# Kernel tuning notes

Hardware: AMD Instinct MI355X
Metric: run time of the kernel (lower is better)

Reference implementation:

```python
import jax, jax.numpy as jnp
import numpy as np

EMBED_DIM = 2048
NUM_HEADS = 16
HEAD_DIM = EMBED_DIM // NUM_HEADS


def setup_inputs() -> dict:
    key = jax.random.key(0)
    k1, k2, k3, k4 = jax.random.split(key, 4)
    x = jax.random.normal(k1, (4, 2048, EMBED_DIM), dtype=jnp.float32)
    # torch nn.Linear weight shape: [out_features, in_features]
    W_qkv = jax.random.normal(k2, (3 * EMBED_DIM, EMBED_DIM), dtype=jnp.float32) * (EMBED_DIM ** -0.5)
    W_out = jax.random.normal(k3, (EMBED_DIM, EMBED_DIM), dtype=jnp.float32) * (EMBED_DIM ** -0.5)
    b_out = jax.random.normal(k4, (EMBED_DIM,), dtype=jnp.float32) * 0.01
    return {"x": x, "W_qkv": W_qkv, "W_out": W_out, "b_out": b_out}


def reference(x, W_qkv, W_out, b_out):
    B, S, E = x.shape
    H, D = NUM_HEADS, HEAD_DIM
    qkv = jnp.einsum('bse,fe->bsf', x, W_qkv)            # [B,S,3E]
    q, k, v = jnp.split(qkv, 3, axis=-1)
    # [B,S,E] -> [B,H,S,D]
    q = q.reshape(B, S, H, D).transpose(0, 2, 1, 3)
    k = k.reshape(B, S, H, D).transpose(0, 2, 1, 3)
    v = v.reshape(B, S, H, D).transpose(0, 2, 1, 3)
    scale = D ** -0.5
    scores = jnp.einsum('bhqd,bhkd->bhqk', q, k) * scale  # [B,H,S,S]
    attn = jax.nn.softmax(scores, axis=-1)
    out = jnp.einsum('bhqk,bhkd->bhqd', attn, v)          # [B,H,S,D]
    out = out.transpose(0, 2, 1, 3).reshape(B, S, E)
    return jnp.einsum('bse,fe->bsf', out, W_out) + b_out
```

## Files before the change

### kernel.cpp

```cpp
#include <hip/hip_runtime.h>
#include <stdint.h>
#include <stddef.h>

#define BATCH 4
#define SEQ   2048
#define EDIM  2048
#define NH    16
#define HD    128
#define MTOT  (BATCH*SEQ)

#define QSCALE (0.08838834764831845f * 1.4426950408889634f)

typedef __bf16 bf16_t;
typedef __attribute__((ext_vector_type(8))) __bf16 bf16x8;
typedef __attribute__((ext_vector_type(4))) __bf16 bf16x4;
typedef __attribute__((ext_vector_type(4))) float f32x4;
typedef __attribute__((ext_vector_type(16))) float f32x16;
typedef __attribute__((ext_vector_type(2))) unsigned int uint32x2;

#define GLD16(l, g) __builtin_amdgcn_global_load_lds( \
    (const uint32_t __attribute__((address_space(1)))*)(g), \
    (uint32_t __attribute__((address_space(3)))*)(l), 16, 0, 0)

#define RAW_BARRIER()  asm volatile("s_barrier" ::: "memory")
#define WAITCNT_VM(n)  asm volatile("s_waitcnt vmcnt(" #n ")" ::: "memory")

__global__ void cast_bf16_kernel(const float* __restrict__ in,
                                 bf16_t* __restrict__ out, int n4) {
    int i = blockIdx.x * blockDim.x + threadIdx.x;
    if (i < n4) {
        float4 v = ((const float4*)in)[i];
        bf16x4 o = { (__bf16)v.x, (__bf16)v.y, (__bf16)v.z, (__bf16)v.w };
        ((bf16x4*)out)[i] = o;
    }
}

template<int EPI>
__global__ __launch_bounds__(256)
void gemm_nt(const bf16_t* __restrict__ A, const bf16_t* __restrict__ B,
             int M, int N, int K,
             float* __restrict__ outf, const float* __restrict__ bias,
             bf16_t* __restrict__ qb, bf16_t* __restrict__ kb,
             bf16_t* __restrict__ vb)
{
    __shared__ bf16_t As[128*64];
    __shared__ bf16_t Bs[128*64];
    const int tid  = threadIdx.x;
    const int lane = tid & 63;
    const int l15  = lane & 15;
    const int quad = lane >> 4;
    const int wave = tid >> 6;
    const int wm = (wave & 1) * 64;
    const int wn = (wave >> 1) * 64;
    const int bm = blockIdx.x * 128;
    const int bn = blockIdx.y * 128;

    f32x4 acc[4][4] = {};

    for (int k0 = 0; k0 < K; k0 += 64) {
#pragma unroll
        for (int i = 0; i < 4; i++) {
            int lin = i*2048 + tid*8;
            int row = lin >> 6;
            int c   = (lin >> 3) & 7;
            int scol = (c ^ (row & 7)) * 8;
            GLD16(&As[lin], A + (long)(bm + row)*K + k0 + scol);
            GLD16(&Bs[lin], B + (long)(bn + row)*K + k0 + scol);
        }
        __syncthreads();
#pragma unroll
        for (int kk = 0; kk < 2; kk++) {
            bf16x8 af[4], bfr[4];
#pragma unroll
            for (int mt = 0; mt < 4; mt++)
                af[mt] = *(const bf16x8*)&As[(wm + mt*16 + l15)*64 +
                                             (((kk*4 + quad) ^ (l15 & 7)) * 8)];
#pragma unroll
            for (int nt = 0; nt < 4; nt++)
                bfr[nt] = *(const bf16x8*)&Bs[(wn + nt*16 + l15)*64 +
                                              (((kk*4 + quad) ^ (l15 & 7)) * 8)];
#pragma unroll
            for (int mt = 0; mt < 4; mt++)
#pragma unroll
                for (int nt = 0; nt < 4; nt++)
                    acc[mt][nt] = __builtin_amdgcn_mfma_f32_16x16x32_bf16(
                        af[mt], bfr[nt], acc[mt][nt], 0, 0, 0);
        }
        __syncthreads();
    }

    if (EPI == 0) {
#pragma unroll
        for (int nt = 0; nt < 4; nt++) {
            int colg = bn + wn + nt*16 + l15;
            int which = colg >> 11;
            int e = colg & 2047;
            int h = e >> 7, d = e & 127;
#pragma unroll
            for (int mt = 0; mt < 4; mt++) {
#pragma unroll
                for (int r = 0; r < 4; r++) {
                    int rowg = bm + wm + mt*16 + quad*4 + r;
                    int b = rowg >> 11, s = rowg & 2047;
                    long bh = (long)b*NH + h;
                    if (which == 0)
                        qb[(bh*SEQ + s)*HD + d] = (__bf16)(acc[mt][nt][r] * QSCALE);
                    else if (which == 1)
                        kb[(bh*SEQ + s)*HD + d] = (__bf16)acc[mt][nt][r];
                    else
                        vb[(bh*HD + d)*SEQ + s] = (__bf16)acc[mt][nt][r];
                }
            }
        }
    } else {
#pragma unroll
        for (int nt = 0; nt < 4; nt++) {
            int colg = bn + wn + nt*16 + l15;
            float bv = bias[colg];
#pragma unroll
            for (int mt = 0; mt < 4; mt++)
#pragma unroll
                for (int r = 0; r < 4; r++) {
                    int rowg = bm + wm + mt*16 + quad*4 + r;
                    outf[(long)rowg*EDIM + colg] = acc[mt][nt][r] + bv;
                }
        }
    }
}

__device__ __forceinline__ void pswap(uint32_t& x, uint32_t& y) {
    uint32x2 r = __builtin_amdgcn_permlane32_swap(x, y, false, false);
    x = r[0]; y = r[1];
}
__device__ __forceinline__ uint32_t pkbf16(float a, float b) {
    union { uint32_t u; __bf16 h[2]; } w;
    w.h[0] = (__bf16)a; w.h[1] = (__bf16)b;
    return w.u;
}
__device__ __forceinline__ float xswap_max(float v) {
    union { float f; uint32_t u; } a, b;
    a.f = v; b.f = v;
    pswap(a.u, b.u);
    return fmaxf(a.f, b.f);
}
__device__ __forceinline__ float xswap_add(float v) {
    union { float f; uint32_t u; } a, b;
    a.f = v; b.f = v;
    pswap(a.u, b.u);
    return a.f + b.f;
}

template<int B>
__device__ __forceinline__ bf16x8 mkfrag(f32x16 p) {
    uint32_t w0 = pkbf16(p[B+0], p[B+1]);
    uint32_t w2 = pkbf16(p[B+4], p[B+5]);
    pswap(w0, w2);
    uint32_t w1 = pkbf16(p[B+2], p[B+3]);
    uint32_t w3 = pkbf16(p[B+6], p[B+7]);
    pswap(w1, w3);
    union { uint32_t u[4]; bf16x8 v; } r;
    r.u[0] = w0; r.u[1] = w1; r.u[2] = w2; r.u[3] = w3;
    return r.v;
}

__global__ __launch_bounds__(512, 2)
void attn_kernel(const bf16_t* __restrict__ qb, const bf16_t* __restrict__ kb,
                 const bf16_t* __restrict__ vb, bf16_t* __restrict__ ob)
{
    __shared__ bf16_t SM[32768];
    bf16_t* const K0 = SM;
    bf16_t* const K1 = SM + 8192;
    bf16_t* const V0 = SM + 16384;
    bf16_t* const V1 = SM + 24576;

    const int tid  = threadIdx.x;
    const int lane = tid & 63;
    const int l31  = lane & 31;
    const int l15  = lane & 15;
    const int l7   = lane & 7;
    const int hi   = lane >> 5;
    const int warp = tid >> 6;

    const int bh = blockIdx.x & 63;
    const int q0 = (blockIdx.x >> 6) * 256;
    const int b  = bh >> 4;
    const int h  = bh & 15;

    const bf16_t* kg0 = kb + (long)bh*SEQ*HD;
    const bf16_t* vg0 = vb + (long)bh*HD*SEQ;

    bf16x8 qf[8];
    {
        const bf16_t* qg = qb + ((long)bh*SEQ + q0 + warp*32 + l31)*HD + hi*8;
#pragma unroll
        for (int ds = 0; ds < 8; ds++)
            qf[ds] = *(const bf16x8*)(qg + ds*16);
    }

#pragma unroll
    for (int i = 0; i < 2; i++) {
        int lin = i*4096 + tid*8;
        { int row = lin >> 7, c = (lin >> 3) & 15;
          GLD16(&K0[lin], kg0 + (long)row*HD + ((c ^ (row & 15)) * 8)); }
        { int row = lin >> 6, c = (lin >> 3) & 7;
          GLD16(&V0[lin], vg0 + (long)row*SEQ + ((c ^ (row & 7)) * 8)); }
    }

    f32x16 oacc[4] = {};
    float m = -1e30f, lsum = 0.f;

    const int NT = SEQ / 64;
    for (int t = 0; t < NT; t++) {
        bf16_t* const Kc = (t & 1) ? K1 : K0;
        bf16_t* const Vc = (t & 1) ? V1 : V0;
        bf16_t* const Kn = (t & 1) ? K0 : K1;
        bf16_t* const Vn = (t & 1) ? V0 : V1;

        RAW_BARRIER();
        {
            int tn = (t + 1 == NT) ? 0 : t + 1;
            const bf16_t* kg = kg0 + (long)tn*64*HD;
            const bf16_t* vg = vg0 + tn*64;
#pragma unroll
            for (int i = 0; i < 2; i++) {
                int lin = i*4096 + tid*8;
                { int row = lin >> 7, c = (lin >> 3) & 15;
                  GLD16(&Kn[lin], kg + (long)row*HD + ((c ^ (row & 15)) * 8)); }
                { int row = lin >> 6, c = (lin >> 3) & 7;
                  GLD16(&Vn[lin], vg + (long)row*SEQ + ((c ^ (row & 7)) * 8)); }
            }
        }
        WAITCNT_VM(4);
        RAW_BARRIER();

        f32x16 p0 = {}, p1 = {};
        __builtin_amdgcn_s_setprio(1);
#pragma unroll
        for (int ds = 0; ds < 8; ds++) {
            const int sc = ((ds*2 + hi) ^ l15) * 8;
            bf16x8 kf0 = *(const bf16x8*)&Kc[l31*128 + sc];
            bf16x8 kf1 = *(const bf16x8*)&Kc[(32 + l31)*128 + sc];
            p0 = __builtin_amdgcn_mfma_f32_32x32x16_bf16(kf0, qf[ds], p0, 0, 0, 0);
            p1 = __builtin_amdgcn_mfma_f32_32x32x16_bf16(kf1, qf[ds], p1, 0, 0, 0);
        }
        __builtin_amdgcn_s_setprio(0);

        float mx;
        {
            float tm[8];
#pragma unroll
            for (int r = 0; r < 8; r++)
                tm[r] = fmaxf(fmaxf(p0[r], p0[r+8]), fmaxf(p1[r], p1[r+8]));
#pragma unroll
            for (int s2 = 4; s2 > 0; s2 >>= 1)
#pragma unroll
                for (int r = 0; r < s2; r++) tm[r] = fmaxf(tm[r], tm[r+s2]);
            mx = xswap_max(tm[0]);
        }
        float mo = m;
        float mn = fmaxf(mo, mx);
        m = mn;
        if (__any(mn > mo)) {
            float av = exp2f(mo - mn);
            lsum *= av;
#pragma unroll
            for (int d = 0; d < 4; d++)
#pragma unroll
                for (int r = 0; r < 16; r++) oacc[d][r] *= av;
        }
#pragma unroll
        for (int r = 0; r < 16; r++) p0[r] = exp2f(p0[r] - mn);
#pragma unroll
        for (int r = 0; r < 16; r++) p1[r] = exp2f(p1[r] - mn);
        {
            float ts[8];
#pragma unroll
            for (int r = 0; r < 8; r++)
                ts[r] = (p0[r] + p0[r+8]) + (p1[r] + p1[r+8]);
#pragma unroll
            for (int s2 = 4; s2 > 0; s2 >>= 1)
#pragma unroll
                for (int r = 0; r < s2; r++) ts[r] += ts[r+s2];
            lsum += xswap_add(ts[0]);
        }

        bf16x8 pf0 = mkfrag<0>(p0);
        bf16x8 pf1 = mkfrag<8>(p0);
        bf16x8 pf2 = mkfrag<0>(p1);
        bf16x8 pf3 = mkfrag<8>(p1);
        __builtin_amdgcn_s_setprio(1);
#pragma unroll
        for (int d = 0; d < 4; d++) {
            bf16x8 vf0 = *(const bf16x8*)&Vc[(d*32 + l31)*64 + (((0 + hi) ^ l7) * 8)];
            oacc[d] = __builtin_amdgcn_mfma_f32_32x32x16_bf16(vf0, pf0, oacc[d], 0, 0, 0);
            bf16x8 vf1 = *(const bf16x8*)&Vc[(d*32 + l31)*64 + (((2 + hi) ^ l7) * 8)];
            oacc[d] = __builtin_amdgcn_mfma_f32_32x32x16_bf16(vf1, pf1, oacc[d], 0, 0, 0);
            bf16x8 vf2 = *(const bf16x8*)&Vc[(d*32 + l31)*64 + (((4 + hi) ^ l7) * 8)];
            oacc[d] = __builtin_amdgcn_mfma_f32_32x32x16_bf16(vf2, pf2, oacc[d], 0, 0, 0);
            bf16x8 vf3 = *(const bf16x8*)&Vc[(d*32 + l31)*64 + (((6 + hi) ^ l7) * 8)];
            oacc[d] = __builtin_amdgcn_mfma_f32_32x32x16_bf16(vf3, pf3, oacc[d], 0, 0, 0);
        }
        __builtin_amdgcn_s_setprio(0);
    }

    {
        float inv = 1.0f / lsum;
        long obase = ((long)b*SEQ + q0 + warp*32 + l31)*EDIM + h*HD + hi*8;
#pragma unroll
        for (int d = 0; d < 4; d++) {
            f32x16 o;
#pragma unroll
            for (int r = 0; r < 16; r++) o[r] = oacc[d][r] * inv;
            bf16x8 f0 = mkfrag<0>(o);
            bf16x8 f1 = mkfrag<8>(o);
            *(bf16x8*)&ob[obase + d*32]      = f0;
            *(bf16x8*)&ob[obase + d*32 + 16] = f1;
        }
    }
}

extern "C" void kernel_launch(void* const* d_in, const int* in_sizes, int n_in,
                              void* d_out, int out_size, void* d_ws, size_t ws_size,
                              hipStream_t stream) {
    const float* x    = (const float*)d_in[0];
    const float* wqkv = (const float*)d_in[1];
    const float* wout = (const float*)d_in[2];
    const float* bout = (const float*)d_in[3];
    float* out = (float*)d_out;

    char* w = (char*)d_ws;
    bf16_t* xb    = (bf16_t*)w; w += (size_t)MTOT*EDIM*2;
    bf16_t* wqkvb = (bf16_t*)w; w += (size_t)3*EDIM*EDIM*2;
    bf16_t* woutb = (bf16_t*)w; w += (size_t)EDIM*EDIM*2;
    bf16_t* qbuf  = (bf16_t*)w; w += (size_t)MTOT*EDIM*2;
    bf16_t* kbuf  = (bf16_t*)w; w += (size_t)MTOT*EDIM*2;
    bf16_t* vbuf  = (bf16_t*)w; w += (size_t)MTOT*EDIM*2;
    bf16_t* attnb = (bf16_t*)w; w += (size_t)MTOT*EDIM*2;

    cast_bf16_kernel<<<MTOT*EDIM/1024, 256, 0, stream>>>(x, xb, MTOT*EDIM/4);
    cast_bf16_kernel<<<3*EDIM*EDIM/1024, 256, 0, stream>>>(wqkv, wqkvb, 3*EDIM*EDIM/4);
    cast_bf16_kernel<<<EDIM*EDIM/1024, 256, 0, stream>>>(wout, woutb, EDIM*EDIM/4);

    gemm_nt<0><<<dim3(MTOT/128, 3*EDIM/128), 256, 0, stream>>>(
        xb, wqkvb, MTOT, 3*EDIM, EDIM, nullptr, nullptr, qbuf, kbuf, vbuf);

    attn_kernel<<<dim3(512), 512, 0, stream>>>(qbuf, kbuf, vbuf, attnb);

    gemm_nt<1><<<dim3(MTOT/128, EDIM/128), 256, 0, stream>>>(
        attnb, woutb, MTOT, EDIM, EDIM, out, bout, nullptr, nullptr, nullptr);
}
```

Before: 676.0 us.

## Rewrite GEMM as 256x256 double-buffered pipelined kernel with block swizzle

Both projection GEMMs move from 128x128 tiles with single-buffered LDS and 256 threads to 256x256 tiles with 512 threads, double-buffered LDS, and four quarter-tile MFMA phases interleaved with async global-to-LDS loads for the next K step. The idea is to hide global load latency behind MFMA work, raise arithmetic intensity per tile, and improve L2 reuse through an XCD-aware block index swizzle. It adds s_setprio around MFMA bursts and raw barriers with manual vmcnt waits. The cost is higher register and LDS use (128KB of LDS per block), so only one block fits per CU despite the launch bounds asking for two, and the hand-counted waitcnt synchronization is fragile.

```diff
diff --git a/kernel.cpp b/kernel.cpp
--- a/kernel.cpp
+++ b/kernel.cpp
@@ -35,74 +35,129 @@
     }
 }
 
+#define STAGE_A(dst, src, bm_, k0_, h) do { \
+  _Pragma("unroll") \
+  for (int i_ = 0; i_ < 2; i_++) { \
+    int idx_ = i_*512 + tid; \
+    int lr_ = idx_ >> 3, c_ = idx_ & 7; \
+    int gr_ = (lr_ & 63) + ((lr_ & 64) << 1) + (h)*64; \
+    GLD16(&(dst)[gr_*64 + c_*8], \
+          (src) + ((bm_) + gr_)*(long)K + (k0_) + ((c_ ^ (gr_ & 7)) * 8)); \
+  } } while (0)
+
+#define STAGE_B(dst, src, bn_, k0_, h) do { \
+  _Pragma("unroll") \
+  for (int i_ = 0; i_ < 2; i_++) { \
+    int idx_ = i_*512 + tid; \
+    int lr_ = idx_ >> 3, c_ = idx_ & 7; \
+    int gr_ = (lr_ & 31) + ((lr_ >> 5) << 6) + (h)*32; \
+    GLD16(&(dst)[gr_*64 + c_*8], \
+          (src) + ((bn_) + gr_)*(long)K + (k0_) + ((c_ ^ (gr_ & 7)) * 8)); \
+  } } while (0)
+
+#define READ_A(MB) do { \
+  _Pragma("unroll") for (int mt_ = 0; mt_ < 4; mt_++) \
+  _Pragma("unroll") for (int kk_ = 0; kk_ < 2; kk_++) \
+    a[mt_][kk_] = *(const bf16x8*)&Ac[(wm + (MB)*64 + mt_*16 + l15)*64 + \
+                                      (((kk_*4 + quad) ^ (l15 & 7)) * 8)]; } while (0)
+
+#define READ_B(NB) do { \
+  _Pragma("unroll") for (int nt_ = 0; nt_ < 2; nt_++) \
+  _Pragma("unroll") for (int kk_ = 0; kk_ < 2; kk_++) \
+    b[(NB)*2 + nt_][kk_] = *(const bf16x8*)&Bc[(wn + (NB)*32 + nt_*16 + l15)*64 + \
+                                               (((kk_*4 + quad) ^ (l15 & 7)) * 8)]; } while (0)
+
+#define MFMA_Q(MB, NB) do { \
+  __builtin_amdgcn_s_setprio(1); \
+  _Pragma("unroll") for (int mt_ = 0; mt_ < 4; mt_++) \
+  _Pragma("unroll") for (int nt_ = 0; nt_ < 2; nt_++) \
+  _Pragma("unroll") for (int kk_ = 0; kk_ < 2; kk_++) \
+    acc[(MB)*4 + mt_][(NB)*2 + nt_] = __builtin_amdgcn_mfma_f32_16x16x32_bf16( \
+        a[mt_][kk_], b[(NB)*2 + nt_][kk_], acc[(MB)*4 + mt_][(NB)*2 + nt_], 0, 0, 0); \
+  __builtin_amdgcn_s_setprio(0); } while (0)
+
 template<int EPI>
-__global__ __launch_bounds__(256)
+__global__ __launch_bounds__(512, 2)
 void gemm_nt(const bf16_t* __restrict__ A, const bf16_t* __restrict__ B,
              int M, int N, int K,
              float* __restrict__ outf, const float* __restrict__ bias,
              bf16_t* __restrict__ qb, bf16_t* __restrict__ kb,
              bf16_t* __restrict__ vb)
 {
-    __shared__ bf16_t As[128*64];
-    __shared__ bf16_t Bs[128*64];
+    __shared__ bf16_t SA[2][256*64];
+    __shared__ bf16_t SB[2][256*64];
     const int tid  = threadIdx.x;
     const int lane = tid & 63;
     const int l15  = lane & 15;
     const int quad = lane >> 4;
     const int wave = tid >> 6;
-    const int wm = (wave & 1) * 64;
-    const int wn = (wave >> 1) * 64;
-    const int bm = blockIdx.x * 128;
-    const int bn = blockIdx.y * 128;
-
-    f32x4 acc[4][4] = {};
-
-    for (int k0 = 0; k0 < K; k0 += 64) {
-#pragma unroll
-        for (int i = 0; i < 4; i++) {
-            int lin = i*2048 + tid*8;
-            int row = lin >> 6;
-            int c   = (lin >> 3) & 7;
-            int scol = (c ^ (row & 7)) * 8;
-            GLD16(&As[lin], A + (long)(bm + row)*K + k0 + scol);
-            GLD16(&Bs[lin], B + (long)(bn + row)*K + k0 + scol);
-        }
-        __syncthreads();
-#pragma unroll
-        for (int kk = 0; kk < 2; kk++) {
-            bf16x8 af[4], bfr[4];
-#pragma unroll
-            for (int mt = 0; mt < 4; mt++)
-                af[mt] = *(const bf16x8*)&As[(wm + mt*16 + l15)*64 +
-                                             (((kk*4 + quad) ^ (l15 & 7)) * 8)];
-#pragma unroll
-            for (int nt = 0; nt < 4; nt++)
-                bfr[nt] = *(const bf16x8*)&Bs[(wn + nt*16 + l15)*64 +
-                                              (((kk*4 + quad) ^ (l15 & 7)) * 8)];
-#pragma unroll
-            for (int mt = 0; mt < 4; mt++)
-#pragma unroll
-                for (int nt = 0; nt < 4; nt++)
-                    acc[mt][nt] = __builtin_amdgcn_mfma_f32_16x16x32_bf16(
-                        af[mt], bfr[nt], acc[mt][nt], 0, 0, 0);
-        }
-        __syncthreads();
+    const int wm = (wave >> 2) * 128;
+    const int wn = (wave & 3) * 64;
+
+    const int nbx = M >> 8;
+    const int cpx = gridDim.x >> 3;
+    const int bid = blockIdx.x;
+    const int swz = (bid & 7) * cpx + (bid >> 3);
+    const long bm = (long)(swz % nbx) * 256;
+    const long bn = (long)(swz / nbx) * 256;
+
+    f32x4 acc[8][4] = {};
+    bf16x8 a[4][2], b[4][2];
+
+    const int NT = K >> 6;
+
+    STAGE_A(SA[0], A, bm, 0, 0);
+    STAGE_B(SB[0], B, bn, 0, 0);
+    STAGE_B(SB[0], B, bn, 0, 1);
+    STAGE_A(SA[0], A, bm, 0, 1);
+    WAITCNT_VM(4);
+    RAW_BARRIER();
+
+    for (int t = 0; t < NT; t++) {
+        bf16_t* const Ac = SA[t & 1];
+        bf16_t* const Bc = SB[t & 1];
+        bf16_t* const An = SA[(t & 1) ^ 1];
+        bf16_t* const Bn = SB[(t & 1) ^ 1];
+        const long kn = (t + 1 == NT) ? 0 : (long)(t + 1) * 64;
+
+        READ_A(0); READ_B(0);
+        STAGE_A(An, A, bm, kn, 0);
+        WAITCNT_VM(4);
+        RAW_BARRIER();
+        MFMA_Q(0, 0);
+        RAW_BARRIER();
+        READ_B(1);
+        STAGE_B(Bn, B, bn, kn, 0);
+        WAITCNT_VM(4);
+        RAW_BARRIER();
+        MFMA_Q(0, 1);
+        RAW_BARRIER();
+        READ_A(1);
+        STAGE_B(Bn, B, bn, kn, 1);
+        RAW_BARRIER();
+        MFMA_Q(1, 1);
+        RAW_BARRIER();
+        STAGE_A(An, A, bm, kn, 1);
+        WAITCNT_VM(4);
+        RAW_BARRIER();
+        MFMA_Q(1, 0);
+        RAW_BARRIER();
     }
 
     if (EPI == 0) {
 #pragma unroll
         for (int nt = 0; nt < 4; nt++) {
-            int colg = bn + wn + nt*16 + l15;
+            int colg = (int)bn + wn + nt*16 + l15;
             int which = colg >> 11;
             int e = colg & 2047;
             int h = e >> 7, d = e & 127;
 #pragma unroll
-            for (int mt = 0; mt < 4; mt++) {
+            for (int mt = 0; mt < 8; mt++) {
 #pragma unroll
                 for (int r = 0; r < 4; r++) {
-                    int rowg = bm + wm + mt*16 + quad*4 + r;
-                    int b = rowg >> 11, s = rowg & 2047;
-                    long bh = (long)b*NH + h;
+                    int rowg = (int)bm + wm + mt*16 + quad*4 + r;
+                    int bb = rowg >> 11, s = rowg & 2047;
+                    long bh = (long)bb*NH + h;
                     if (which == 0)
                         qb[(bh*SEQ + s)*HD + d] = (__bf16)(acc[mt][nt][r] * QSCALE);
                     else if (which == 1)
@@ -115,13 +170,13 @@
     } else {
 #pragma unroll
         for (int nt = 0; nt < 4; nt++) {
-            int colg = bn + wn + nt*16 + l15;
+            int colg = (int)bn + wn + nt*16 + l15;
             float bv = bias[colg];
 #pragma unroll
-            for (int mt = 0; mt < 4; mt++)
+            for (int mt = 0; mt < 8; mt++)
 #pragma unroll
                 for (int r = 0; r < 4; r++) {
-                    int rowg = bm + wm + mt*16 + quad*4 + r;
+                    int rowg = (int)bm + wm + mt*16 + quad*4 + r;
                     outf[(long)rowg*EDIM + colg] = acc[mt][nt][r] + bv;
                 }
         }
@@ -341,11 +396,11 @@
     cast_bf16_kernel<<<3*EDIM*EDIM/1024, 256, 0, stream>>>(wqkv, wqkvb, 3*EDIM*EDIM/4);
     cast_bf16_kernel<<<EDIM*EDIM/1024, 256, 0, stream>>>(wout, woutb, EDIM*EDIM/4);
 
-    gemm_nt<0><<<dim3(MTOT/128, 3*EDIM/128), 256, 0, stream>>>(
+    gemm_nt<0><<<dim3((MTOT/256)*(3*EDIM/256)), 512, 0, stream>>>(
         xb, wqkvb, MTOT, 3*EDIM, EDIM, nullptr, nullptr, qbuf, kbuf, vbuf);
 
     attn_kernel<<<dim3(512), 512, 0, stream>>>(qbuf, kbuf, vbuf, attnb);
 
-    gemm_nt<1><<<dim3(MTOT/128, EDIM/128), 256, 0, stream>>>(
+    gemm_nt<1><<<dim3((MTOT/256)*(EDIM/256)), 512, 0, stream>>>(
         attnb, woutb, MTOT, EDIM, EDIM, out, bout, nullptr, nullptr, nullptr);
 }
```

Result: slower. 691.5 us (+2.3%).
